# Optimization experiments

Hardware: AMD Instinct MI355X
Metric: run time of the kernel (lower is better)

The kernel has to match this reference:

```python
import jax, jax.numpy as jnp
import numpy as np

N = 16777216  # batch*A*width*height (flat anchor-score vector)
BINS = 10
LOSS_WEIGHT = 1.0


def setup_inputs() -> dict:
    key = jax.random.key(0)
    k1, k2, k3 = jax.random.split(key, 3)
    pred = jax.random.normal(k1, (N,), dtype=jnp.float32)          # IoU logits
    target = jax.random.uniform(k2, (N,), dtype=jnp.float32)       # IoU targets in [0,1]
    label_weight = (jax.random.uniform(k3, (N,)) > 0.3).astype(jnp.float32)  # 1=valid, 0=ignore
    return {"pred": pred, "target": target, "label_weight": label_weight, "bins": BINS}


def reference(pred, target, label_weight, bins):
    # target is detached in the original module
    target = jax.lax.stop_gradient(target)
    # gradient norm g = |sigmoid(pred).detach() - target|, lies in [0,1]
    g = jnp.abs(jax.lax.stop_gradient(jax.nn.sigmoid(pred)) - target)
    valid = label_weight > 0
    validf = valid.astype(jnp.float32)
    tot = jnp.maximum(jnp.sum(validf), 1.0)

    # edges are i/bins with last edge nudged by 1e-6, so bin = floor(g*bins) clipped to bins-1
    bin_idx = jnp.clip((g * bins).astype(jnp.int32), 0, bins - 1)
    counts = jax.ops.segment_sum(validf, bin_idx, num_segments=bins)  # per-bin valid counts
    n = jnp.sum(counts > 0).astype(jnp.float32)                        # number of nonempty bins
    counts_safe = jnp.maximum(counts, 1.0)
    w_per_bin = jnp.where(counts > 0, tot / counts_safe, 0.0) / jnp.maximum(n, 1.0)
    weights = jnp.where(valid, w_per_bin[bin_idx], 0.0)

    # weighted BCE-with-logits, reduction='sum', stable form: logaddexp(0,x) - x*z
    bce = jnp.logaddexp(0.0, pred) - pred * target
    loss = jnp.sum(weights * bce) / tot
    return loss * LOSS_WEIGHT
```

## Files before the change

### kernel.cpp

```cpp
#include <hip/hip_runtime.h>

#define BINS 10
#define REPLICAS 16
#define NBLOCKS 2048
#define NTHREADS 256


typedef float vfloat4 __attribute__((ext_vector_type(4)));

__global__ __launch_bounds__(NTHREADS, 4)
void ghm_pass1(const float* __restrict__ pred,
               const float* __restrict__ target,
               const float* __restrict__ lw,
               float* __restrict__ rep_sums,
               unsigned int* __restrict__ rep_cnts,
               int n)
{
    __shared__ float ls[BINS];
    __shared__ unsigned int lc[BINS];
    if (threadIdx.x < BINS) { ls[threadIdx.x] = 0.0f; lc[threadIdx.x] = 0u; }

    float s0=0.f,s1=0.f,s2=0.f,s3=0.f,s4=0.f,s5=0.f,s6=0.f,s7=0.f,s8=0.f,s9=0.f;
    unsigned long long cpk = 0ull;

#define SBIN(B, S) { (S) += (bi_ == (B)) ? bce_ : 0.0f; }
#define PROC(P, T, W) do {                                                     \
    float p_ = (P), t_ = (T);                                                  \
    float ap_ = fabsf(p_);                                                     \
    float q_  = __builtin_amdgcn_exp2f(ap_ * -1.4426950408889634f); \
    float r_  = __builtin_amdgcn_rcpf(1.0f + q_);                              \
    float sig_ = (p_ >= 0.0f) ? r_ : (1.0f - r_);                              \
    float g_   = fabsf(sig_ - t_);                                             \
    int bi_ = (int)(g_ * 10.0f);                                               \
    bi_ = bi_ > 9 ? 9 : bi_;                                                   \
    bi_ = ((W) > 0.0f) ? bi_ : 10;              \
    float bce_ = fmaxf(p_, 0.0f)                                               \
               + 0.6931471805599453f * __builtin_amdgcn_logf(1.0f + q_)        \
               - p_ * t_;                                                      \
    cpk += 1ull << (6 * bi_);                                                  \
    SBIN(0,s0) SBIN(1,s1) SBIN(2,s2) SBIN(3,s3) SBIN(4,s4)                     \
    SBIN(5,s5) SBIN(6,s6) SBIN(7,s7) SBIN(8,s8) SBIN(9,s9)                     \
} while (0)
#define PROC4(PV, TV, WV) {                                                    \
    PROC((PV).x, (TV).x, (WV).x);                                              \
    PROC((PV).y, (TV).y, (WV).y);                                              \
    PROC((PV).z, (TV).z, (WV).z);                                              \
    PROC((PV).w, (TV).w, (WV).w); }

    const int n4 = n >> 2;
    const int full = n4 / (NBLOCKS * NTHREADS);
    const vfloat4* p4 = (const vfloat4*)pred;
    const vfloat4* t4 = (const vfloat4*)target;
    const vfloat4* w4 = (const vfloat4*)lw;

    if (full >= 2) {
        const int base = blockIdx.x * full * NTHREADS + threadIdx.x;
        vfloat4 pA = __builtin_nontemporal_load(&p4[base]);
        vfloat4 tA = __builtin_nontemporal_load(&t4[base]);
        vfloat4 wA = __builtin_nontemporal_load(&w4[base]);
        vfloat4 pB = __builtin_nontemporal_load(&p4[base + NTHREADS]);
        vfloat4 tB = __builtin_nontemporal_load(&t4[base + NTHREADS]);
        vfloat4 wB = __builtin_nontemporal_load(&w4[base + NTHREADS]);
        __builtin_amdgcn_sched_barrier(0);
        for (int j = 2; j < full; ++j) {
            const int idx = base + j * NTHREADS;
            vfloat4 pC = __builtin_nontemporal_load(&p4[idx]);
            vfloat4 tC = __builtin_nontemporal_load(&t4[idx]);
            vfloat4 wC = __builtin_nontemporal_load(&w4[idx]);
            __builtin_amdgcn_sched_barrier(0);
            PROC4(pA, tA, wA);
            pA = pB; tA = tB; wA = wB;
            pB = pC; tB = tC; wB = wC;
        }
        PROC4(pA, tA, wA);
        PROC4(pB, tB, wB);
    }
    const int gid = blockIdx.x * NTHREADS + threadIdx.x;
    const int stride = NBLOCKS * NTHREADS;
    for (int i = full * stride + gid; i < n4; i += stride) {
        vfloat4 pv = p4[i], tv = t4[i], wv = w4[i];
        PROC4(pv, tv, wv);
    }
    for (int j = (n4 << 2) + gid; j < n; j += stride) {
        PROC(pred[j], target[j], lw[j]);
    }

    unsigned int c0 = (unsigned int)(cpk       ) & 63u;
    unsigned int c1 = (unsigned int)(cpk >>  6 ) & 63u;
    unsigned int c2 = (unsigned int)(cpk >> 12 ) & 63u;
    unsigned int c3 = (unsigned int)(cpk >> 18 ) & 63u;
    unsigned int c4 = (unsigned int)(cpk >> 24 ) & 63u;
    unsigned int c5 = (unsigned int)(cpk >> 30 ) & 63u;
    unsigned int c6 = (unsigned int)(cpk >> 36 ) & 63u;
    unsigned int c7 = (unsigned int)(cpk >> 42 ) & 63u;
    unsigned int c8 = (unsigned int)(cpk >> 48 ) & 63u;
    unsigned int c9 = (unsigned int)(cpk >> 54 ) & 63u;

#define WREDUCE(S, C) {                                                        \
    _Pragma("unroll")                                                          \
    for (int o_ = 32; o_ > 0; o_ >>= 1) {                                      \
        (S) += __shfl_down((S), o_, 64);                                       \
        (C) += __shfl_down((C), o_, 64);                                       \
    } }
    WREDUCE(s0,c0) WREDUCE(s1,c1) WREDUCE(s2,c2) WREDUCE(s3,c3) WREDUCE(s4,c4)
    WREDUCE(s5,c5) WREDUCE(s6,c6) WREDUCE(s7,c7) WREDUCE(s8,c8) WREDUCE(s9,c9)

    __syncthreads();
    if ((threadIdx.x & 63) == 0) {
        atomicAdd(&ls[0], s0); atomicAdd(&lc[0], c0);
        atomicAdd(&ls[1], s1); atomicAdd(&lc[1], c1);
        atomicAdd(&ls[2], s2); atomicAdd(&lc[2], c2);
        atomicAdd(&ls[3], s3); atomicAdd(&lc[3], c3);
        atomicAdd(&ls[4], s4); atomicAdd(&lc[4], c4);
        atomicAdd(&ls[5], s5); atomicAdd(&lc[5], c5);
        atomicAdd(&ls[6], s6); atomicAdd(&lc[6], c6);
        atomicAdd(&ls[7], s7); atomicAdd(&lc[7], c7);
        atomicAdd(&ls[8], s8); atomicAdd(&lc[8], c8);
        atomicAdd(&ls[9], s9); atomicAdd(&lc[9], c9);
    }
    __syncthreads();
    if (threadIdx.x < BINS) {
        int rep = blockIdx.x & (REPLICAS - 1);
        atomicAdd(&rep_sums[rep * BINS + threadIdx.x], ls[threadIdx.x]);
        atomicAdd(&rep_cnts[rep * BINS + threadIdx.x], lc[threadIdx.x]);
    }
#undef PROC
#undef PROC4
#undef SBIN
#undef WREDUCE
}

__global__ void ghm_finalize(const float* __restrict__ rep_sums,
                             const unsigned int* __restrict__ rep_cnts,
                             float* __restrict__ out)
{
    __shared__ double S[BINS];
    __shared__ unsigned int C[BINS];
    int t = threadIdx.x;
    if (t < BINS) {
        double s = 0.0;
        unsigned int cc = 0u;
        for (int r = 0; r < REPLICAS; ++r) {
            s += (double)rep_sums[r * BINS + t];
            cc += rep_cnts[r * BINS + t];
        }
        S[t] = s;
        C[t] = cc;
    }
    __syncthreads();
    if (t == 0) {
        double n_ne = 0.0;
        for (int b = 0; b < BINS; ++b) if (C[b] > 0u) n_ne += 1.0;
        double nn = n_ne > 1.0 ? n_ne : 1.0;
        double loss = 0.0;
        for (int b = 0; b < BINS; ++b)
            if (C[b] > 0u) loss += S[b] / ((double)C[b] * nn);
        out[0] = (float)loss;
    }
}

extern "C" void kernel_launch(void* const* d_in, const int* in_sizes, int n_in,
                              void* d_out, int out_size, void* d_ws, size_t ws_size,
                              hipStream_t stream)
{
    const float* pred = (const float*)d_in[0];
    const float* target = (const float*)d_in[1];
    const float* lw = (const float*)d_in[2];
    int n = in_sizes[0];

    float* rep_sums = (float*)d_ws;
    unsigned int* rep_cnts =
        (unsigned int*)((char*)d_ws + REPLICAS * BINS * sizeof(float));

    (void)hipMemsetAsync(d_ws, 0, 2 * REPLICAS * BINS * sizeof(float), stream);
    ghm_pass1<<<NBLOCKS, NTHREADS, 0, stream>>>(pred, target, lw,
                                                rep_sums, rep_cnts, n);
    ghm_finalize<<<1, 64, 0, stream>>>(rep_sums, rep_cnts, (float*)d_out);
}
```

Baseline: 184.9 us.

## Replace per-bin register accumulators with lane-sliced LDS atomic histogram

```diff
diff --git a/kernel.cpp b/kernel.cpp
--- a/kernel.cpp
+++ b/kernel.cpp
@@ -4,6 +4,7 @@
 #define REPLICAS 16
 #define NBLOCKS 2048
 #define NTHREADS 256
+#define SLOTS 64
 
 
 typedef float vfloat4 __attribute__((ext_vector_type(4)));
@@ -13,34 +14,33 @@
                const float* __restrict__ target,
                const float* __restrict__ lw,
                float* __restrict__ rep_sums,
-               unsigned int* __restrict__ rep_cnts,
+               float* __restrict__ rep_cnts,
                int n)
 {
-    __shared__ float ls[BINS];
-    __shared__ unsigned int lc[BINS];
-    if (threadIdx.x < BINS) { ls[threadIdx.x] = 0.0f; lc[threadIdx.x] = 0u; }
+    __shared__ float lsbuf[2 * BINS * SLOTS];
+    #pragma unroll
+    for (int i = threadIdx.x; i < 2 * BINS * SLOTS; i += NTHREADS) lsbuf[i] = 0.0f;
+    __syncthreads();
 
-    float s0=0.f,s1=0.f,s2=0.f,s3=0.f,s4=0.f,s5=0.f,s6=0.f,s7=0.f,s8=0.f,s9=0.f;
-    unsigned long long cpk = 0ull;
+    float* myls = &lsbuf[threadIdx.x & 63];
 
-#define SBIN(B, S) { (S) += (bi_ == (B)) ? bce_ : 0.0f; }
 #define PROC(P, T, W) do {                                                     \
-    float p_ = (P), t_ = (T);                                                  \
-    float ap_ = fabsf(p_);                                                     \
-    float q_  = __builtin_amdgcn_exp2f(ap_ * -1.4426950408889634f); \
-    float r_  = __builtin_amdgcn_rcpf(1.0f + q_);                              \
+    float p_ = (P), t_ = (T), w_ = (W);                                        \
+    float q_ = __builtin_amdgcn_exp2f(fabsf(p_) * -1.4426950408889634f);       \
+    float d_ = 1.0f + q_;                                                      \
+    float r_ = __builtin_amdgcn_rcpf(d_);                                      \
     float sig_ = (p_ >= 0.0f) ? r_ : (1.0f - r_);                              \
-    float g_   = fabsf(sig_ - t_);                                             \
-    int bi_ = (int)(g_ * 10.0f);                                               \
+    int bi_ = (int)(fabsf(sig_ - t_) * 10.0f);                                 \
     bi_ = bi_ > 9 ? 9 : bi_;                                                   \
-    bi_ = ((W) > 0.0f) ? bi_ : 10;              \
     float bce_ = fmaxf(p_, 0.0f)                                               \
-               + 0.6931471805599453f * __builtin_amdgcn_logf(1.0f + q_)        \
+               + 0.6931471805599453f * __builtin_amdgcn_logf(d_)               \
                - p_ * t_;                                                      \
-    cpk += 1ull << (6 * bi_);                                                  \
-    SBIN(0,s0) SBIN(1,s1) SBIN(2,s2) SBIN(3,s3) SBIN(4,s4)                     \
-    SBIN(5,s5) SBIN(6,s6) SBIN(7,s7) SBIN(8,s8) SBIN(9,s9)                     \
+    bool v_ = (w_ > 0.0f);                                                     \
+    float* slot_ = myls + (bi_ << 6);                                          \
+    unsafeAtomicAdd(slot_, v_ ? bce_ : 0.0f);                                  \
+    unsafeAtomicAdd(slot_ + BINS * SLOTS, v_ ? 1.0f : 0.0f);                   \
 } while (0)
+
 #define PROC4(PV, TV, WV) {                                                    \
     PROC((PV).x, (TV).x, (WV).x);                                              \
     PROC((PV).y, (TV).y, (WV).y);                                              \
@@ -48,113 +48,96 @@
     PROC((PV).w, (TV).w, (WV).w); }
 
     const int n4 = n >> 2;
-    const int full = n4 / (NBLOCKS * NTHREADS);
+    const int stride = NBLOCKS * NTHREADS;
+    const int gid = blockIdx.x * NTHREADS + threadIdx.x;
+    const int full = n4 / stride;
     const vfloat4* p4 = (const vfloat4*)pred;
     const vfloat4* t4 = (const vfloat4*)target;
     const vfloat4* w4 = (const vfloat4*)lw;
 
-    if (full >= 2) {
-        const int base = blockIdx.x * full * NTHREADS + threadIdx.x;
-        vfloat4 pA = __builtin_nontemporal_load(&p4[base]);
-        vfloat4 tA = __builtin_nontemporal_load(&t4[base]);
-        vfloat4 wA = __builtin_nontemporal_load(&w4[base]);
-        vfloat4 pB = __builtin_nontemporal_load(&p4[base + NTHREADS]);
-        vfloat4 tB = __builtin_nontemporal_load(&t4[base + NTHREADS]);
-        vfloat4 wB = __builtin_nontemporal_load(&w4[base + NTHREADS]);
-        __builtin_amdgcn_sched_barrier(0);
-        for (int j = 2; j < full; ++j) {
-            const int idx = base + j * NTHREADS;
-            vfloat4 pC = __builtin_nontemporal_load(&p4[idx]);
-            vfloat4 tC = __builtin_nontemporal_load(&t4[idx]);
-            vfloat4 wC = __builtin_nontemporal_load(&w4[idx]);
-            __builtin_amdgcn_sched_barrier(0);
-            PROC4(pA, tA, wA);
-            pA = pB; tA = tB; wA = wB;
-            pB = pC; tB = tC; wB = wC;
+#define NT(x) __builtin_nontemporal_load(x)
+#define SB    __builtin_amdgcn_sched_barrier(0)
+#define LOADI(K)                                                               \
+    vfloat4 pv##K = NT(&p4[base + (K) * NTHREADS]);                            \
+    vfloat4 tv##K = NT(&t4[base + (K) * NTHREADS]);                            \
+    vfloat4 wv##K = NT(&w4[base + (K) * NTHREADS]);
+
+    if (full == 8) {
+        const int base = blockIdx.x * 8 * NTHREADS + threadIdx.x;
+        LOADI(0) LOADI(1) LOADI(2) SB;
+        PROC4(pv0, tv0, wv0) LOADI(3) SB;
+        PROC4(pv1, tv1, wv1) LOADI(4) SB;
+        PROC4(pv2, tv2, wv2) LOADI(5) SB;
+        PROC4(pv3, tv3, wv3) LOADI(6) SB;
+        PROC4(pv4, tv4, wv4) LOADI(7) SB;
+        PROC4(pv5, tv5, wv5)
+        PROC4(pv6, tv6, wv6)
+        PROC4(pv7, tv7, wv7)
+        for (int i = 8 * stride + gid; i < n4; i += stride) {
+            vfloat4 pv = p4[i], tv = t4[i], wv = w4[i];
+            PROC4(pv, tv, wv);
         }
-        PROC4(pA, tA, wA);
-        PROC4(pB, tB, wB);
+    } else {
+        for (int i = gid; i < n4; i += stride) {
+            vfloat4 pv = p4[i], tv = t4[i], wv = w4[i];
+            PROC4(pv, tv, wv);
+        }
     }
-    const int gid = blockIdx.x * NTHREADS + threadIdx.x;
-    const int stride = NBLOCKS * NTHREADS;
-    for (int i = full * stride + gid; i < n4; i += stride) {
-        vfloat4 pv = p4[i], tv = t4[i], wv = w4[i];
-        PROC4(pv, tv, wv);
-    }
-    for (int j = (n4 << 2) + gid; j < n; j += stride) {
+    for (int j = (n4 << 2) + gid; j < n; j += stride)
         PROC(pred[j], target[j], lw[j]);
-    }
-
-    unsigned int c0 = (unsigned int)(cpk       ) & 63u;
-    unsigned int c1 = (unsigned int)(cpk >>  6 ) & 63u;
-    unsigned int c2 = (unsigned int)(cpk >> 12 ) & 63u;
-    unsigned int c3 = (unsigned int)(cpk >> 18 ) & 63u;
-    unsigned int c4 = (unsigned int)(cpk >> 24 ) & 63u;
-    unsigned int c5 = (unsigned int)(cpk >> 30 ) & 63u;
-    unsigned int c6 = (unsigned int)(cpk >> 36 ) & 63u;
-    unsigned int c7 = (unsigned int)(cpk >> 42 ) & 63u;
-    unsigned int c8 = (unsigned int)(cpk >> 48 ) & 63u;
-    unsigned int c9 = (unsigned int)(cpk >> 54 ) & 63u;
-
-#define WREDUCE(S, C) {                                                        \
-    _Pragma("unroll")                                                          \
-    for (int o_ = 32; o_ > 0; o_ >>= 1) {                                      \
-        (S) += __shfl_down((S), o_, 64);                                       \
-        (C) += __shfl_down((C), o_, 64);                                       \
-    } }
-    WREDUCE(s0,c0) WREDUCE(s1,c1) WREDUCE(s2,c2) WREDUCE(s3,c3) WREDUCE(s4,c4)
-    WREDUCE(s5,c5) WREDUCE(s6,c6) WREDUCE(s7,c7) WREDUCE(s8,c8) WREDUCE(s9,c9)
 
     __syncthreads();
-    if ((threadIdx.x & 63) == 0) {
-        atomicAdd(&ls[0], s0); atomicAdd(&lc[0], c0);
-        atomicAdd(&ls[1], s1); atomicAdd(&lc[1], c1);
-        atomicAdd(&ls[2], s2); atomicAdd(&lc[2], c2);
-        atomicAdd(&ls[3], s3); atomicAdd(&lc[3], c3);
-        atomicAdd(&ls[4], s4); atomicAdd(&lc[4], c4);
-        atomicAdd(&ls[5], s5); atomicAdd(&lc[5], c5);
-        atomicAdd(&ls[6], s6); atomicAdd(&lc[6], c6);
-        atomicAdd(&ls[7], s7); atomicAdd(&lc[7], c7);
-        atomicAdd(&ls[8], s8); atomicAdd(&lc[8], c8);
-        atomicAdd(&ls[9], s9); atomicAdd(&lc[9], c9);
-    }
-    __syncthreads();
-    if (threadIdx.x < BINS) {
-        int rep = blockIdx.x & (REPLICAS - 1);
-        atomicAdd(&rep_sums[rep * BINS + threadIdx.x], ls[threadIdx.x]);
-        atomicAdd(&rep_cnts[rep * BINS + threadIdx.x], lc[threadIdx.x]);
+    const int wv_ = threadIdx.x >> 6;
+    const int ln_ = threadIdx.x & 63;
+    if (wv_ < 2) {
+        float v[BINS];
+        const int off = wv_ * (BINS * SLOTS);
+        #pragma unroll
+        for (int b = 0; b < BINS; ++b) v[b] = lsbuf[off + (b << 6) + ln_];
+        #pragma unroll
+        for (int b = 0; b < BINS; ++b) {
+            #pragma unroll
+            for (int o = 32; o > 0; o >>= 1) v[b] += __shfl_down(v[b], o, 64);
+        }
+        if (ln_ == 0) {
+            const int rep = blockIdx.x & (REPLICAS - 1);
+            float* dst = (wv_ == 0 ? rep_sums : rep_cnts) + rep * BINS;
+            #pragma unroll
+            for (int b = 0; b < BINS; ++b) unsafeAtomicAdd(&dst[b], v[b]);
+        }
     }
 #undef PROC
 #undef PROC4
-#undef SBIN
-#undef WREDUCE
+#undef NT
+#undef SB
+#undef LOADI
 }
 
 __global__ void ghm_finalize(const float* __restrict__ rep_sums,
-                             const unsigned int* __restrict__ rep_cnts,
+                             const float* __restrict__ rep_cnts,
                              float* __restrict__ out)
 {
     __shared__ double S[BINS];
-    __shared__ unsigned int C[BINS];
+    __shared__ float C[BINS];
     int t = threadIdx.x;
     if (t < BINS) {
         double s = 0.0;
-        unsigned int cc = 0u;
+        float c = 0.0f;
         for (int r = 0; r < REPLICAS; ++r) {
             s += (double)rep_sums[r * BINS + t];
-            cc += rep_cnts[r * BINS + t];
+            c += rep_cnts[r * BINS + t];
         }
         S[t] = s;
-        C[t] = cc;
+        C[t] = c;
     }
     __syncthreads();
     if (t == 0) {
         double n_ne = 0.0;
-        for (int b = 0; b < BINS; ++b) if (C[b] > 0u) n_ne += 1.0;
+        for (int b = 0; b < BINS; ++b) if (C[b] > 0.0f) n_ne += 1.0;
         double nn = n_ne > 1.0 ? n_ne : 1.0;
         double loss = 0.0;
         for (int b = 0; b < BINS; ++b)
-            if (C[b] > 0u) loss += S[b] / ((double)C[b] * nn);
+            if (C[b] > 0.0f) loss += S[b] / ((double)C[b] * nn);
         out[0] = (float)loss;
     }
 }
@@ -169,8 +152,7 @@
     int n = in_sizes[0];
 
     float* rep_sums = (float*)d_ws;
-    unsigned int* rep_cnts =
-        (unsigned int*)((char*)d_ws + REPLICAS * BINS * sizeof(float));
+    float* rep_cnts = (float*)((char*)d_ws + REPLICAS * BINS * sizeof(float));
 
     (void)hipMemsetAsync(d_ws, 0, 2 * REPLICAS * BINS * sizeof(float), stream);
     ghm_pass1<<<NBLOCKS, NTHREADS, 0, stream>>>(pred, target, lw,
```

Result: slower. 328.8 us (+77.8%).
